# Performance work log

Measured on AMD Instinct MI355X. Metric: run time of the kernel, lower is better.

## Reference

```python
import jax, jax.numpy as jnp
import numpy as np

K = 3
VOCAB = 32000
EMBED = 1024
SEQ_LEN = 256
BATCH = 8


def setup_inputs() -> dict:
    key = jax.random.key(0)
    k1, k2, k3 = jax.random.split(key, 3)
    tokens_seq = jax.random.randint(k1, (SEQ_LEN, BATCH), 0, VOCAB, dtype=jnp.int64 if jax.config.jax_enable_x64 else jnp.int32)
    W1 = jax.random.normal(k2, (K * VOCAB, EMBED), dtype=jnp.float32) * 0.02
    b1 = jnp.zeros((EMBED,), dtype=jnp.float32)
    W2 = jax.random.normal(k3, (EMBED, VOCAB), dtype=jnp.float32) * 0.02
    b2 = jnp.zeros((VOCAB,), dtype=jnp.float32)
    return {"tokens_seq": tokens_seq, "W1": W1, "b1": b1, "W2": W2, "b2": b2}


def reference(tokens_seq, W1, b1, W2, b2):
    # tokens_seq: (S, B). Context for position t is [pad...] + tokens[t-K:t] (zeros pad).
    S, B = tokens_seq.shape
    padded = jnp.concatenate([jnp.zeros((K, B), dtype=tokens_seq.dtype), tokens_seq], axis=0)  # (S+K, B)
    # one_hot(context).flatten() @ W1 == sum_j W1_rows[j, context_j]
    W1r = W1.reshape(K, VOCAB, EMBED)  # slot-major flatten order matches F.one_hot(...).flatten()
    h = b1
    for j in range(K):  # K is a small compile-time constant
        ctx_j = padded[j:j + S]           # (S, B): j-th slot of each context window
        h = h + W1r[j][ctx_j]             # gather rows: (S, B, E)
    h = jax.nn.relu(h)
    logits = jnp.einsum('sbe,ev->sbv', h, W2) + b2  # (S, B, V)
    return logits
```

## Files before the change

### kernel.cpp

```cpp
#include <hip/hip_runtime.h>
#include <hip/hip_bf16.h>

#define VOCAB 32000
#define EMBED 1024
#define SEQ 256
#define BATCH 8
#define ROWS (SEQ * BATCH)

#define BM 256
#define BN 256
#define BK 64
#define NT (EMBED / BK)

typedef short short8 __attribute__((ext_vector_type(8)));
typedef float f32x4 __attribute__((ext_vector_type(4)));

__device__ __forceinline__ unsigned short f2bf(float f) {
    __hip_bfloat16 h = __float2bfloat16(f);
    return *reinterpret_cast<unsigned short*>(&h);
}

#define GLOAD_LDS16(gsrc, ldst)                                                        \
    __builtin_amdgcn_global_load_lds((const __attribute__((address_space(1))) void*)(gsrc), \
                                     (__attribute__((address_space(3))) void*)(ldst), 16, 0, 0)

__global__ __launch_bounds__(256) void embed_relu_k(const int* __restrict__ toks,
                                                    const float* __restrict__ W1,
                                                    const float* __restrict__ b1,
                                                    unsigned short* __restrict__ h) {
    int r = blockIdx.x;
    int s = r >> 3, b = r & 7;
    int t0 = (s >= 3) ? toks[(s - 3) * BATCH + b] : 0;
    int t1 = (s >= 2) ? toks[(s - 2) * BATCH + b] : 0;
    int t2 = (s >= 1) ? toks[(s - 1) * BATCH + b] : 0;
    int e = threadIdx.x * 4;
    float4 vb = *(const float4*)(b1 + e);
    float4 v0 = *(const float4*)(W1 + ((size_t)0 * VOCAB + t0) * EMBED + e);
    float4 v1 = *(const float4*)(W1 + ((size_t)1 * VOCAB + t1) * EMBED + e);
    float4 v2 = *(const float4*)(W1 + ((size_t)2 * VOCAB + t2) * EMBED + e);
    float x0 = fmaxf(vb.x + v0.x + v1.x + v2.x, 0.0f);
    float x1 = fmaxf(vb.y + v0.y + v1.y + v2.y, 0.0f);
    float x2 = fmaxf(vb.z + v0.z + v1.z + v2.z, 0.0f);
    float x3 = fmaxf(vb.w + v0.w + v1.w + v2.w, 0.0f);
    union { unsigned short u[4]; uint2 v; } o;
    o.u[0] = f2bf(x0); o.u[1] = f2bf(x1); o.u[2] = f2bf(x2); o.u[3] = f2bf(x3);
    *(uint2*)(h + (size_t)r * EMBED + e) = o.v;
}

__global__ __launch_bounds__(256) void w2_conv_t_k(const float* __restrict__ W2,
                                                   unsigned short* __restrict__ W2t) {
    __shared__ float tile[64][65];
    int n0 = blockIdx.x * 64;
    int k0 = blockIdx.y * 64;
    int t = threadIdx.x;
    int tx = t & 15, ty = t >> 4;
#pragma unroll
    for (int p = 0; p < 4; ++p) {
        int k = ty + p * 16;
        float4 v = *(const float4*)(W2 + (size_t)(k0 + k) * VOCAB + n0 + tx * 4);
        tile[k][tx * 4 + 0] = v.x; tile[k][tx * 4 + 1] = v.y;
        tile[k][tx * 4 + 2] = v.z; tile[k][tx * 4 + 3] = v.w;
    }
    __syncthreads();
    int kx = t & 15, ny = t >> 4;
#pragma unroll
    for (int p = 0; p < 4; ++p) {
        int n = ny + p * 16;
        int k = kx * 4;
        union { unsigned short u[4]; uint2 v; } o;
        o.u[0] = f2bf(tile[k + 0][n]); o.u[1] = f2bf(tile[k + 1][n]);
        o.u[2] = f2bf(tile[k + 2][n]); o.u[3] = f2bf(tile[k + 3][n]);
        *(uint2*)(W2t + (size_t)(n0 + n) * EMBED + k0 + k) = o.v;
    }
}

__global__ __launch_bounds__(512, 2) void gemm8_k(const unsigned short* __restrict__ A,
                                                  const unsigned short* __restrict__ B,
                                                  const float* __restrict__ b2,
                                                  float* __restrict__ out) {
    extern __shared__ char lds[];
    char* Al = lds;
    char* Bl = lds + 65536;

    int wg = blockIdx.x;
    int wgid = (wg & 7) * 125 + (wg >> 3);
    int m0 = (wgid & 7) * BM;
    int n0 = (wgid >> 3) * BN;

    int tid = threadIdx.x;
    int w = tid >> 6, lane = tid & 63;
    int wm = w >> 2, wn = w & 3;
    int ksw = ((lane & 7) ^ ((lane >> 3) & 7)) * 8;

    f32x4 acc[8][4] = {};
    short8 af[2][2], bfr[4][2];

    auto stage = [&](const unsigned short* __restrict__ g, int grow0, char* ldsbase, int t) {
#pragma unroll
        for (int j = 0; j < 2; ++j) {
            int c = j * 8 + w;
            int row = c * 8 + (lane >> 3);
            const unsigned short* src = g + (size_t)(grow0 + row) * EMBED + t * BK + ksw;
            GLOAD_LDS16(src, ldsbase + c * 1024);
        }
    };
    auto stA = [&](int buf, int h, int t) { stage(A, m0 + h * 128, Al + buf * 32768 + h * 16384, t); };
    auto stB = [&](int buf, int h, int t) { stage(B, n0 + h * 128, Bl + buf * 32768 + h * 16384, t); };

    auto ldA = [&](int buf, int q) {
#pragma unroll
        for (int i = 0; i < 2; ++i)
#pragma unroll
            for (int kk = 0; kk < 2; ++kk) {
                int row = wm * 128 + (q * 2 + i) * 16 + (lane & 15);
                int cb = ((lane >> 4) * 16 + kk * 64) ^ ((lane & 7) << 4);
                af[i][kk] = *(const short8*)(Al + buf * 32768 + row * 128 + cb);
            }
    };
    auto ldB = [&](int buf) {
#pragma unroll
        for (int n = 0; n < 4; ++n)
#pragma unroll
            for (int kk = 0; kk < 2; ++kk) {
                int row = wn * 64 + n * 16 + (lane & 15);
                int cb = ((lane >> 4) * 16 + kk * 64) ^ ((lane & 7) << 4);
                bfr[n][kk] = *(const short8*)(Bl + buf * 32768 + row * 128 + cb);
            }
    };

    stA(0, 0, 0); stA(0, 1, 0); stB(0, 0, 0); stB(0, 1, 0);
    stB(1, 0, 1); stB(1, 1, 1);
    asm volatile("s_waitcnt vmcnt(4)");
    __builtin_amdgcn_s_barrier();

#define MFMA_Q(q)                                                                             \
    __builtin_amdgcn_s_setprio(1);                                                            \
    _Pragma("unroll") for (int i = 0; i < 2; ++i)                                             \
        _Pragma("unroll") for (int n = 0; n < 4; ++n)                                         \
            _Pragma("unroll") for (int kk = 0; kk < 2; ++kk)                                  \
                acc[(q)*2 + i][n] = __builtin_amdgcn_mfma_f32_16x16x32_bf16(                  \
                    af[i][kk], bfr[n][kk], acc[(q)*2 + i][n], 0, 0, 0);                       \
    __builtin_amdgcn_s_setprio(0);

#define PH(ldbuf, q, DO_LDB, STAGE_STMT, WAITV)                                               \
    ldA(ldbuf, q);                                                                            \
    if (DO_LDB) ldB(ldbuf);                                                                   \
    STAGE_STMT;                                                                               \
    if (DO_LDB) asm volatile("s_waitcnt lgkmcnt(8)");                                         \
    if (WAITV) asm volatile("s_waitcnt vmcnt(4)");                                            \
    __builtin_amdgcn_s_barrier();                                                             \
    asm volatile("s_waitcnt lgkmcnt(0)");                                                     \
    MFMA_Q(q);                                                                                \
    __builtin_amdgcn_s_barrier();

    for (int it = 0; it < NT / 2; ++it) {
        int t1 = (it * 2 + 1) & (NT - 1);
        int t2 = (it * 2 + 2) & (NT - 1);
        int t3 = (it * 2 + 3) & (NT - 1);
        PH(0, 0, true,  stA(1, 0, t1), false)
        PH(0, 1, false, stA(1, 1, t1), false)
        PH(0, 2, false, stB(0, 0, t2), false)
        PH(0, 3, false, stB(0, 1, t2), true)
        PH(1, 0, true,  stA(0, 0, t2), false)
        PH(1, 1, false, stA(0, 1, t2), false)
        PH(1, 2, false, stB(1, 0, t3), false)
        PH(1, 3, false, stB(1, 1, t3), true)
    }
#undef PH
#undef MFMA_Q

    int colq = lane & 15;
    int rowq = (lane >> 4) * 4;
#pragma unroll
    for (int nf = 0; nf < 4; ++nf) {
        int col = n0 + wn * 64 + nf * 16 + colq;
        float bias = b2[col];
#pragma unroll
        for (int mf = 0; mf < 8; ++mf) {
            int row0 = m0 + wm * 128 + mf * 16 + rowq;
#pragma unroll
            for (int q = 0; q < 4; ++q)
                out[(size_t)(row0 + q) * VOCAB + col] = acc[mf][nf][q] + bias;
        }
    }
}

__global__ __launch_bounds__(256) void gemm_k(const unsigned short* __restrict__ h,
                                              const unsigned short* __restrict__ W2t,
                                              const float* __restrict__ b2,
                                              float* __restrict__ out) {
    __shared__ unsigned short Alds[128 * 64];
    __shared__ unsigned short Blds[128 * 64];
    int m0 = blockIdx.x * 128;
    int n0 = blockIdx.y * 128;
    int tid = threadIdx.x;
    int wave = tid >> 6, lane = tid & 63;
    int wr = (wave >> 1) * 64;
    int wc = (wave & 1) * 64;
    int lrow = lane & 15;
    int khalf = (lane >> 4) * 8;
    f32x4 acc[4][4] = {};
    for (int kt = 0; kt < EMBED; kt += 64) {
#pragma unroll
        for (int i = 0; i < 4; ++i) {
            int base = (wave * 4 + i) * 1024;
            int lin = base + lane * 16;
            int row = lin >> 7;
            int colu = (lin & 127) >> 1;
            GLOAD_LDS16(h + (size_t)(m0 + row) * EMBED + kt + colu, (char*)Alds + base);
            GLOAD_LDS16(W2t + (size_t)(n0 + row) * EMBED + kt + colu, (char*)Blds + base);
        }
        __syncthreads();
#pragma unroll
        for (int kc = 0; kc < 2; ++kc) {
            short8 af[4], bf[4];
#pragma unroll
            for (int m = 0; m < 4; ++m)
                af[m] = *(const short8*)(Alds + (wr + m * 16 + lrow) * 64 + kc * 32 + khalf);
#pragma unroll
            for (int n = 0; n < 4; ++n)
                bf[n] = *(const short8*)(Blds + (wc + n * 16 + lrow) * 64 + kc * 32 + khalf);
#pragma unroll
            for (int m = 0; m < 4; ++m)
#pragma unroll
                for (int n = 0; n < 4; ++n)
                    acc[m][n] = __builtin_amdgcn_mfma_f32_16x16x32_bf16(af[m], bf[n], acc[m][n], 0, 0, 0);
        }
        __syncthreads();
    }
    int colq = lane & 15;
    int rowq = (lane >> 4) * 4;
#pragma unroll
    for (int m = 0; m < 4; ++m)
#pragma unroll
        for (int n = 0; n < 4; ++n) {
            int col = n0 + wc + n * 16 + colq;
            float bias = b2[col];
#pragma unroll
            for (int q = 0; q < 4; ++q)
                out[(size_t)(m0 + wr + m * 16 + rowq + q) * VOCAB + col] = acc[m][n][q] + bias;
        }
}

__global__ __launch_bounds__(256) void naive_k(const int* __restrict__ toks,
                                               const float* __restrict__ W1,
                                               const float* __restrict__ b1,
                                               const float* __restrict__ W2,
                                               const float* __restrict__ b2,
                                               float* __restrict__ out) {
    __shared__ float hs[8][1024];
    int r0 = blockIdx.x * 8;
    int e = threadIdx.x * 4;
    for (int rr = 0; rr < 8; ++rr) {
        int r = r0 + rr, s = r >> 3, b = r & 7;
        int t0 = (s >= 3) ? toks[(s - 3) * BATCH + b] : 0;
        int t1 = (s >= 2) ? toks[(s - 2) * BATCH + b] : 0;
        int t2 = (s >= 1) ? toks[(s - 1) * BATCH + b] : 0;
        float4 vb = *(const float4*)(b1 + e);
        float4 v0 = *(const float4*)(W1 + ((size_t)t0) * EMBED + e);
        float4 v1 = *(const float4*)(W1 + ((size_t)VOCAB + t1) * EMBED + e);
        float4 v2 = *(const float4*)(W1 + ((size_t)2 * VOCAB + t2) * EMBED + e);
        hs[rr][e + 0] = fmaxf(vb.x + v0.x + v1.x + v2.x, 0.0f);
        hs[rr][e + 1] = fmaxf(vb.y + v0.y + v1.y + v2.y, 0.0f);
        hs[rr][e + 2] = fmaxf(vb.z + v0.z + v1.z + v2.z, 0.0f);
        hs[rr][e + 3] = fmaxf(vb.w + v0.w + v1.w + v2.w, 0.0f);
    }
    __syncthreads();
    for (int v = threadIdx.x; v < VOCAB; v += 256) {
        float acc[8];
#pragma unroll
        for (int i = 0; i < 8; ++i) acc[i] = b2[v];
        for (int ee = 0; ee < EMBED; ++ee) {
            float wv = W2[(size_t)ee * VOCAB + v];
#pragma unroll
            for (int i = 0; i < 8; ++i) acc[i] += hs[i][ee] * wv;
        }
#pragma unroll
        for (int i = 0; i < 8; ++i) out[(size_t)(r0 + i) * VOCAB + v] = acc[i];
    }
}

extern "C" void kernel_launch(void* const* d_in, const int* in_sizes, int n_in,
                              void* d_out, int out_size, void* d_ws, size_t ws_size,
                              hipStream_t stream) {
    const int* toks = (const int*)d_in[0];
    const float* W1 = (const float*)d_in[1];
    const float* b1 = (const float*)d_in[2];
    const float* W2 = (const float*)d_in[3];
    const float* b2 = (const float*)d_in[4];
    float* out = (float*)d_out;

    const size_t h_bytes = (size_t)ROWS * EMBED * 2;
    const size_t w2t_bytes = (size_t)VOCAB * EMBED * 2;
    if (ws_size >= h_bytes + w2t_bytes) {
        unsigned short* h = (unsigned short*)d_ws;
        unsigned short* W2t = (unsigned short*)((char*)d_ws + h_bytes);
        embed_relu_k<<<ROWS, 256, 0, stream>>>(toks, W1, b1, h);
        w2_conv_t_k<<<dim3(VOCAB / 64, EMBED / 64), 256, 0, stream>>>(W2, W2t);
        hipError_t e = hipFuncSetAttribute(reinterpret_cast<const void*>(gemm8_k),
                                           hipFuncAttributeMaxDynamicSharedMemorySize, 131072);
        if (e == hipSuccess) {
            gemm8_k<<<(ROWS / BM) * (VOCAB / BN), 512, 131072, stream>>>(h, W2t, b2, out);
        } else {
            gemm_k<<<dim3(ROWS / 128, VOCAB / 128), 256, 0, stream>>>(h, W2t, b2, out);
        }
    } else {
        naive_k<<<ROWS / 8, 256, 0, stream>>>(toks, W1, b1, W2, b2, out);
    }
}
```

Measured before the change: 217.4 us.

## Merge prep kernels and make each GEMM block compute two M tiles

The embedding/ReLU kernel and the W2 transpose/convert kernel are merged into one launch, saving a kernel launch and its tail. The main GEMM grid is halved: each workgroup now processes two 256-row M tiles sequentially for the same N tile. It prefetches the second tile's A data while the first tile's epilogue stores run, and the XCD-aware block mapping is recomputed for 500 workgroups. This aims to reuse the B tile and overlap epilogue stores with loads, at the cost of fewer workgroups (500 over 256 CUs at 2 per CU) and longer per-block serial work.

After: 205.6 us. 5.4% less time.

```diff
diff --git a/kernel.cpp b/kernel.cpp
--- a/kernel.cpp
+++ b/kernel.cpp
@@ -24,53 +24,55 @@
     __builtin_amdgcn_global_load_lds((const __attribute__((address_space(1))) void*)(gsrc), \
                                      (__attribute__((address_space(3))) void*)(ldst), 16, 0, 0)
 
-__global__ __launch_bounds__(256) void embed_relu_k(const int* __restrict__ toks,
-                                                    const float* __restrict__ W1,
-                                                    const float* __restrict__ b1,
-                                                    unsigned short* __restrict__ h) {
-    int r = blockIdx.x;
-    int s = r >> 3, b = r & 7;
-    int t0 = (s >= 3) ? toks[(s - 3) * BATCH + b] : 0;
-    int t1 = (s >= 2) ? toks[(s - 2) * BATCH + b] : 0;
-    int t2 = (s >= 1) ? toks[(s - 1) * BATCH + b] : 0;
-    int e = threadIdx.x * 4;
-    float4 vb = *(const float4*)(b1 + e);
-    float4 v0 = *(const float4*)(W1 + ((size_t)0 * VOCAB + t0) * EMBED + e);
-    float4 v1 = *(const float4*)(W1 + ((size_t)1 * VOCAB + t1) * EMBED + e);
-    float4 v2 = *(const float4*)(W1 + ((size_t)2 * VOCAB + t2) * EMBED + e);
-    float x0 = fmaxf(vb.x + v0.x + v1.x + v2.x, 0.0f);
-    float x1 = fmaxf(vb.y + v0.y + v1.y + v2.y, 0.0f);
-    float x2 = fmaxf(vb.z + v0.z + v1.z + v2.z, 0.0f);
-    float x3 = fmaxf(vb.w + v0.w + v1.w + v2.w, 0.0f);
-    union { unsigned short u[4]; uint2 v; } o;
-    o.u[0] = f2bf(x0); o.u[1] = f2bf(x1); o.u[2] = f2bf(x2); o.u[3] = f2bf(x3);
-    *(uint2*)(h + (size_t)r * EMBED + e) = o.v;
-}
-
-__global__ __launch_bounds__(256) void w2_conv_t_k(const float* __restrict__ W2,
-                                                   unsigned short* __restrict__ W2t) {
+__global__ __launch_bounds__(256) void prep_k(const int* __restrict__ toks,
+                                              const float* __restrict__ W1,
+                                              const float* __restrict__ b1,
+                                              const float* __restrict__ W2,
+                                              unsigned short* __restrict__ h,
+                                              unsigned short* __restrict__ W2t) {
     __shared__ float tile[64][65];
-    int n0 = blockIdx.x * 64;
-    int k0 = blockIdx.y * 64;
+    int bid = blockIdx.x;
     int t = threadIdx.x;
-    int tx = t & 15, ty = t >> 4;
-#pragma unroll
-    for (int p = 0; p < 4; ++p) {
-        int k = ty + p * 16;
-        float4 v = *(const float4*)(W2 + (size_t)(k0 + k) * VOCAB + n0 + tx * 4);
-        tile[k][tx * 4 + 0] = v.x; tile[k][tx * 4 + 1] = v.y;
-        tile[k][tx * 4 + 2] = v.z; tile[k][tx * 4 + 3] = v.w;
-    }
-    __syncthreads();
-    int kx = t & 15, ny = t >> 4;
-#pragma unroll
-    for (int p = 0; p < 4; ++p) {
-        int n = ny + p * 16;
-        int k = kx * 4;
+    if (bid < 8000) {
+        int n0 = (bid % 500) * 64;
+        int k0 = (bid / 500) * 64;
+        int tx = t & 15, ty = t >> 4;
+#pragma unroll
+        for (int p = 0; p < 4; ++p) {
+            int k = ty + p * 16;
+            float4 v = *(const float4*)(W2 + (size_t)(k0 + k) * VOCAB + n0 + tx * 4);
+            tile[k][tx * 4 + 0] = v.x; tile[k][tx * 4 + 1] = v.y;
+            tile[k][tx * 4 + 2] = v.z; tile[k][tx * 4 + 3] = v.w;
+        }
+        __syncthreads();
+        int kx = t & 15, ny = t >> 4;
+#pragma unroll
+        for (int p = 0; p < 4; ++p) {
+            int n = ny + p * 16;
+            int k = kx * 4;
+            union { unsigned short u[4]; uint2 v; } o;
+            o.u[0] = f2bf(tile[k + 0][n]); o.u[1] = f2bf(tile[k + 1][n]);
+            o.u[2] = f2bf(tile[k + 2][n]); o.u[3] = f2bf(tile[k + 3][n]);
+            *(uint2*)(W2t + (size_t)(n0 + n) * EMBED + k0 + k) = o.v;
+        }
+    } else {
+        int r = bid - 8000;
+        int s = r >> 3, b = r & 7;
+        int t0 = (s >= 3) ? toks[(s - 3) * BATCH + b] : 0;
+        int t1 = (s >= 2) ? toks[(s - 2) * BATCH + b] : 0;
+        int t2 = (s >= 1) ? toks[(s - 1) * BATCH + b] : 0;
+        int e = t * 4;
+        float4 vb = *(const float4*)(b1 + e);
+        float4 v0 = *(const float4*)(W1 + ((size_t)0 * VOCAB + t0) * EMBED + e);
+        float4 v1 = *(const float4*)(W1 + ((size_t)1 * VOCAB + t1) * EMBED + e);
+        float4 v2 = *(const float4*)(W1 + ((size_t)2 * VOCAB + t2) * EMBED + e);
+        float x0 = fmaxf(vb.x + v0.x + v1.x + v2.x, 0.0f);
+        float x1 = fmaxf(vb.y + v0.y + v1.y + v2.y, 0.0f);
+        float x2 = fmaxf(vb.z + v0.z + v1.z + v2.z, 0.0f);
+        float x3 = fmaxf(vb.w + v0.w + v1.w + v2.w, 0.0f);
         union { unsigned short u[4]; uint2 v; } o;
-        o.u[0] = f2bf(tile[k + 0][n]); o.u[1] = f2bf(tile[k + 1][n]);
-        o.u[2] = f2bf(tile[k + 2][n]); o.u[3] = f2bf(tile[k + 3][n]);
-        *(uint2*)(W2t + (size_t)(n0 + n) * EMBED + k0 + k) = o.v;
+        o.u[0] = f2bf(x0); o.u[1] = f2bf(x1); o.u[2] = f2bf(x2); o.u[3] = f2bf(x3);
+        *(uint2*)(h + (size_t)r * EMBED + e) = o.v;
     }
 }
 
@@ -83,9 +85,11 @@
     char* Bl = lds + 65536;
 
     int wg = blockIdx.x;
-    int wgid = (wg & 7) * 125 + (wg >> 3);
-    int m0 = (wgid & 7) * BM;
-    int n0 = (wgid >> 3) * BN;
+    int xcd = wg & 7, idx = wg >> 3;
+    int wgid = (xcd < 4 ? xcd * 63 : 4 * 63 + (xcd - 4) * 62) + idx;
+    int mg = wgid & 3;
+    int n0 = (wgid >> 2) * BN;
+    int m0 = mg * 512;
 
     int tid = threadIdx.x;
     int w = tid >> 6, lane = tid & 63;
@@ -104,15 +108,15 @@
             GLOAD_LDS16(src, ldsbase + c * 1024);
         }
     };
-    auto stA = [&](int buf, int h, int t) { stage(A, m0 + h * 128, Al + buf * 32768 + h * 16384, t); };
-    auto stB = [&](int buf, int h, int t) { stage(B, n0 + h * 128, Bl + buf * 32768 + h * 16384, t); };
-
-    auto ldA = [&](int buf, int q) {
+    auto stA = [&](int buf, int hh, int t, int mbase) { stage(A, mbase + hh * 128, Al + buf * 32768 + hh * 16384, t); };
+    auto stB = [&](int buf, int hh, int t) { stage(B, n0 + hh * 128, Bl + buf * 32768 + hh * 16384, t); };
+
+    auto ldA = [&](int buf, int qq) {
 #pragma unroll
         for (int i = 0; i < 2; ++i)
 #pragma unroll
             for (int kk = 0; kk < 2; ++kk) {
-                int row = wm * 128 + (q * 2 + i) * 16 + (lane & 15);
+                int row = wm * 128 + (qq * 2 + i) * 16 + (lane & 15);
                 int cb = ((lane >> 4) * 16 + kk * 64) ^ ((lane & 7) << 4);
                 af[i][kk] = *(const short8*)(Al + buf * 32768 + row * 128 + cb);
             }
@@ -127,11 +131,6 @@
                 bfr[n][kk] = *(const short8*)(Bl + buf * 32768 + row * 128 + cb);
             }
     };
-
-    stA(0, 0, 0); stA(0, 1, 0); stB(0, 0, 0); stB(0, 1, 0);
-    stB(1, 0, 1); stB(1, 1, 1);
-    asm volatile("s_waitcnt vmcnt(4)");
-    __builtin_amdgcn_s_barrier();
 
 #define MFMA_Q(q)                                                                             \
     __builtin_amdgcn_s_setprio(1);                                                            \
@@ -153,36 +152,62 @@
     MFMA_Q(q);                                                                                \
     __builtin_amdgcn_s_barrier();
 
-    for (int it = 0; it < NT / 2; ++it) {
-        int t1 = (it * 2 + 1) & (NT - 1);
-        int t2 = (it * 2 + 2) & (NT - 1);
-        int t3 = (it * 2 + 3) & (NT - 1);
-        PH(0, 0, true,  stA(1, 0, t1), false)
-        PH(0, 1, false, stA(1, 1, t1), false)
-        PH(0, 2, false, stB(0, 0, t2), false)
-        PH(0, 3, false, stB(0, 1, t2), true)
-        PH(1, 0, true,  stA(0, 0, t2), false)
-        PH(1, 1, false, stA(0, 1, t2), false)
-        PH(1, 2, false, stB(1, 0, t3), false)
-        PH(1, 3, false, stB(1, 1, t3), true)
-    }
+    auto kloop = [&](int mcur) {
+        for (int it = 0; it < NT / 2; ++it) {
+            int t1 = (it * 2 + 1) & (NT - 1);
+            int t2 = (it * 2 + 2) & (NT - 1);
+            int t3 = (it * 2 + 3) & (NT - 1);
+            PH(0, 0, true,  stA(1, 0, t1, mcur), false)
+            PH(0, 1, false, stA(1, 1, t1, mcur), false)
+            PH(0, 2, false, stB(0, 0, t2),       false)
+            PH(0, 3, false, stB(0, 1, t2),       true)
+            PH(1, 0, true,  stA(0, 0, t2, mcur), false)
+            PH(1, 1, false, stA(0, 1, t2, mcur), false)
+            PH(1, 2, false, stB(1, 0, t3),       false)
+            PH(1, 3, false, stB(1, 1, t3),       true)
+        }
+    };
+
+    int colq = lane & 15;
+    int rowq = (lane >> 4) * 4;
+    auto epi = [&](int mbase) {
+#pragma unroll
+        for (int nf = 0; nf < 4; ++nf) {
+            int col = n0 + wn * 64 + nf * 16 + colq;
+            float bias = b2[col];
+#pragma unroll
+            for (int mf = 0; mf < 8; ++mf) {
+                int row0 = mbase + wm * 128 + mf * 16 + rowq;
+#pragma unroll
+                for (int q = 0; q < 4; ++q)
+                    out[(size_t)(row0 + q) * VOCAB + col] = acc[mf][nf][q] + bias;
+            }
+        }
+    };
+
+    stA(0, 0, 0, m0); stA(0, 1, 0, m0); stB(0, 0, 0); stB(0, 1, 0);
+    stB(1, 0, 1); stB(1, 1, 1);
+    asm volatile("s_waitcnt vmcnt(4)");
+    __builtin_amdgcn_s_barrier();
+
+    kloop(m0);
+
+    int m1 = m0 + 256;
+    stA(0, 0, 0, m1); stA(0, 1, 0, m1);
+    epi(m0);
+    asm volatile("s_waitcnt vmcnt(63)" ::: "memory");
+    __builtin_amdgcn_s_barrier();
+
+#pragma unroll
+    for (int mf = 0; mf < 8; ++mf)
+#pragma unroll
+        for (int nf = 0; nf < 4; ++nf)
+            acc[mf][nf] = f32x4{0.f, 0.f, 0.f, 0.f};
+
+    kloop(m1);
+    epi(m1);
 #undef PH
 #undef MFMA_Q
-
-    int colq = lane & 15;
-    int rowq = (lane >> 4) * 4;
-#pragma unroll
-    for (int nf = 0; nf < 4; ++nf) {
-        int col = n0 + wn * 64 + nf * 16 + colq;
-        float bias = b2[col];
-#pragma unroll
-        for (int mf = 0; mf < 8; ++mf) {
-            int row0 = m0 + wm * 128 + mf * 16 + rowq;
-#pragma unroll
-            for (int q = 0; q < 4; ++q)
-                out[(size_t)(row0 + q) * VOCAB + col] = acc[mf][nf][q] + bias;
-        }
-    }
 }
 
 __global__ __launch_bounds__(256) void gemm_k(const unsigned short* __restrict__ h,
@@ -295,12 +320,11 @@
     if (ws_size >= h_bytes + w2t_bytes) {
         unsigned short* h = (unsigned short*)d_ws;
         unsigned short* W2t = (unsigned short*)((char*)d_ws + h_bytes);
-        embed_relu_k<<<ROWS, 256, 0, stream>>>(toks, W1, b1, h);
-        w2_conv_t_k<<<dim3(VOCAB / 64, EMBED / 64), 256, 0, stream>>>(W2, W2t);
+        prep_k<<<8000 + ROWS, 256, 0, stream>>>(toks, W1, b1, W2, h, W2t);
         hipError_t e = hipFuncSetAttribute(reinterpret_cast<const void*>(gemm8_k),
                                            hipFuncAttributeMaxDynamicSharedMemorySize, 131072);
         if (e == hipSuccess) {
-            gemm8_k<<<(ROWS / BM) * (VOCAB / BN), 512, 131072, stream>>>(h, W2t, b2, out);
+            gemm8_k<<<(ROWS / 512) * (VOCAB / BN), 512, 131072, stream>>>(h, W2t, b2, out);
         } else {
             gemm_k<<<dim3(ROWS / 128, VOCAB / 128), 256, 0, stream>>>(h, W2t, b2, out);
         }
```
